# Kernel tuning notes

Hardware: AMD Instinct MI355X
Metric: run time of the kernel (lower is better)

The kernel has to match this reference:

```python
import jax, jax.numpy as jnp
import numpy as np

D_STATE = 8
HIDDEN = 256


def _neighbor_sum(x):
    # frozen depthwise 3x3 conv, all-ones kernel with zero center, padding=1
    B, C, H, W = x.shape
    xp = jnp.pad(x, ((0, 0), (0, 0), (1, 1), (1, 1)))
    full = sum(xp[:, :, di:di + H, dj:dj + W] for di in range(3) for dj in range(3))
    return full - x  # subtract center tap


def setup_inputs() -> dict:
    key = jax.random.key(0)
    ks = jax.random.split(key, 6)
    B, H, W = 4, 256, 256
    c_in = 2 * D_STATE          # 16
    c_nbr = c_in * 8            # 128
    c_out = 8 * D_STATE         # 64
    s = 0.05
    return {
        "x_cat": jax.random.normal(ks[0], (B, c_in, H, W), dtype=jnp.float32),
        "w1": jax.random.normal(ks[1], (HIDDEN, c_nbr), dtype=jnp.float32) * s,
        "w2": jax.random.normal(ks[2], (HIDDEN, HIDDEN), dtype=jnp.float32) * s,
        "w3": jax.random.normal(ks[3], (HIDDEN, HIDDEN), dtype=jnp.float32) * s,
        "w4": jax.random.normal(ks[4], (HIDDEN, HIDDEN), dtype=jnp.float32) * s,
        "w5": jax.random.normal(ks[5], (c_out, HIDDEN), dtype=jnp.float32) * s,
    }


def reference(x_cat, w1, w2, w3, w4, w5):
    B, C, H, W = x_cat.shape
    d_state = C // 2
    # depthwise stencil: each of the 8 out-channels per group is the same neighbor sum
    nbr = _neighbor_sum(x_cat)                      # [B, 2d, H, W]
    xn = jnp.repeat(nbr, 8, axis=1)                 # [B, 16d, H, W]
    # five 1x1 convs with interleaved ELU (per-pixel MLP)
    h = jax.nn.elu(jnp.einsum('bchw,oc->bohw', xn, w1))
    h = jax.nn.elu(jnp.einsum('bchw,oc->bohw', h, w2))
    h = jax.nn.elu(jnp.einsum('bchw,oc->bohw', h, w3))
    h = jax.nn.elu(jnp.einsum('bchw,oc->bohw', h, w4))
    F_int = jnp.einsum('bchw,oc->bohw', h, w5)      # [B, 8d, H, W]
    d4 = 4 * d_state
    real = F_int[:, :d4].reshape(B, 4, d_state, H, W).mean(axis=1) * 0.1
    imag = F_int[:, d4:].reshape(B, 4, d_state, H, W).mean(axis=1) * 0.1
    return jnp.concatenate([real, imag], axis=1)    # [B, 2d, H, W]
```

## Files before the change

### kernel.cpp

```cpp
#include <hip/hip_runtime.h>

typedef __attribute__((ext_vector_type(8))) short bf16x8;
typedef __attribute__((ext_vector_type(4))) float f32x4;

__device__ __forceinline__ unsigned int f2bf(float f) {
  unsigned int u = __builtin_bit_cast(unsigned int, f);
  return (u + 0x7FFFu + ((u >> 16) & 1u)) >> 16;
}
__device__ __forceinline__ float eluf(float x) {
  return x > 0.f ? x : (__expf(x) - 1.f);
}
__device__ __forceinline__ unsigned int cvt_pk_bf16(float a, float b) {
  unsigned int r;
  asm("v_cvt_pk_bf16_f32 %0, %1, %2" : "=v"(r) : "v"(a), "v"(b));
  return r;
}

__global__ __launch_bounds__(256) void prep_kernel(
    const float* __restrict__ w1, const float* __restrict__ w2,
    const float* __restrict__ w3, const float* __restrict__ w4,
    const float* __restrict__ w5, unsigned short* __restrict__ ws) {
  int idx = blockIdx.x * 256 + threadIdx.x;
  float v = 0.f;
  if (idx < 8192) {
    int mt = idx >> 9, l = (idx >> 3) & 63, j = idx & 7;
    int o = mt * 16 + (l & 15), c = (l >> 4) * 8 + j;
    if (c < 16) {
      const float* r = w1 + o * 128 + c * 8;
      v = ((r[0] + r[1]) + (r[2] + r[3])) + ((r[4] + r[5]) + (r[6] + r[7]));
    }
  } else if (idx < 204800) {
    int t = idx - 8192;
    int which = t >> 16, e = t & 65535;
    const float* w = (which == 0) ? w2 : (which == 1) ? w3 : w4;
    int mt = e >> 12, kt = (e >> 9) & 7, l = (e >> 3) & 63, j = e & 7;
    int o = mt * 16 + (l & 15), c = kt * 32 + (l >> 4) * 8 + j;
    v = w[o * 256 + c];
  } else {
    int e = idx - 204800;
    int kt = e >> 9, l = (e >> 3) & 63, j = e & 7;
    int d = l & 15, c = kt * 32 + (l >> 4) * 8 + j;
    float s = 0.f;
    if (d < 8) {
      for (int g = 0; g < 4; ++g) s += w5[(g * 8 + d) * 256 + c];
    } else {
      for (int g = 0; g < 4; ++g) s += w5[(32 + g * 8 + (d - 8)) * 256 + c];
    }
    v = 0.025f * s;
  }
  ws[idx] = (unsigned short)f2bf(v);
}

#define ACT0 0
#define BUF0 5120
#define BUF1 38912

__global__ __launch_bounds__(256, 2) void qca_kernel(
    const float* __restrict__ xcat, const unsigned short* __restrict__ wsu,
    float* __restrict__ out) {
  __shared__ __align__(16) char lds[72704];
  float* xt = reinterpret_cast<float*>(lds + BUF0);

  const int tid = threadIdx.x;
  const int w = tid >> 6, l = tid & 63;
  const int l15 = l & 15, lhi = l >> 4;

  const int tile = blockIdx.x << 6;
  const int bimg = tile >> 16;
  const int y = (tile >> 8) & 255;
  const int x0 = tile & 255;

  for (int t = tid; t < 16 * 3 * 66; t += 256) {
    int c = t / 198;
    int rem = t - c * 198;
    int rr = rem / 66;
    int xl = rem - rr * 66;
    int gy = y + rr - 1, gx = x0 + xl - 1;
    float v = 0.f;
    if (gy >= 0 && gy < 256 && gx >= 0 && gx < 256)
      v = xcat[(size_t)(bimg * 16 + c) * 65536 + gy * 256 + gx];
    xt[t] = v;
  }
  __syncthreads();

  for (int t = tid; t < 2048; t += 256) {
    int p = t & 63, c = t >> 6;
    float v = 0.f;
    if (c < 16) {
      const float* bp = xt + c * 198 + (p + 1);
      v = (bp[-1] + bp[0] + bp[1]) + (bp[65] + bp[67]) +
          (bp[131] + bp[132] + bp[133]);
    }
    reinterpret_cast<unsigned short*>(lds)[p * 40 + c] = (unsigned short)f2bf(v);
  }
  __syncthreads();

  const int lb_r = l15 * 528 + lhi * 16;
  const int lb_w = l15 * 528 + w * 128 + lhi * 8;
  const int lb_a1 = l15 * 80 + lhi * 16;

  f32x4 acc[4][4];

  auto epi = [&](int dstoff) {
#pragma unroll
    for (int mi = 0; mi < 4; ++mi)
#pragma unroll
      for (int ni = 0; ni < 4; ++ni) {
        f32x4 v = acc[mi][ni];
        unsigned int u01 = cvt_pk_bf16(eluf(v[0]), eluf(v[1]));
        unsigned int u23 = cvt_pk_bf16(eluf(v[2]), eluf(v[3]));
        *reinterpret_cast<uint2*>(lds + lb_w + (dstoff + ni * 8448 + mi * 32)) =
            uint2{u01, u23};
      }
  };

  {
#pragma unroll
    for (int mi = 0; mi < 4; ++mi)
#pragma unroll
      for (int ni = 0; ni < 4; ++ni) acc[mi][ni] = f32x4{0.f, 0.f, 0.f, 0.f};
    const bf16x8* w1v = reinterpret_cast<const bf16x8*>(wsu);
    bf16x8 a[4], bq[4];
#pragma unroll
    for (int mi = 0; mi < 4; ++mi) a[mi] = w1v[((w << 2) + mi) * 64 + l];
#pragma unroll
    for (int ni = 0; ni < 4; ++ni)
      bq[ni] = *reinterpret_cast<const bf16x8*>(lds + lb_a1 + ni * 1280);
#pragma unroll
    for (int mi = 0; mi < 4; ++mi)
#pragma unroll
      for (int ni = 0; ni < 4; ++ni)
        acc[mi][ni] = __builtin_amdgcn_mfma_f32_16x16x32_bf16(
            a[mi], bq[ni], acc[mi][ni], 0, 0, 0);
    epi(BUF1);
    __syncthreads();
  }

  auto mid = [&](int srcoff, int dstoff, const unsigned short* wbase) {
    const bf16x8* wv = reinterpret_cast<const bf16x8*>(wbase);
#pragma unroll
    for (int mi = 0; mi < 4; ++mi)
#pragma unroll
      for (int ni = 0; ni < 4; ++ni) acc[mi][ni] = f32x4{0.f, 0.f, 0.f, 0.f};
#pragma unroll
    for (int kt = 0; kt < 8; ++kt) {
      bf16x8 a[4], bq[4];
#pragma unroll
      for (int mi = 0; mi < 4; ++mi)
        a[mi] = wv[(((w << 2) + mi) * 8 + kt) * 64 + l];
#pragma unroll
      for (int ni = 0; ni < 4; ++ni)
        bq[ni] = *reinterpret_cast<const bf16x8*>(
            lds + lb_r + (srcoff + ni * 8448 + kt * 64));
#pragma unroll
      for (int mi = 0; mi < 4; ++mi)
#pragma unroll
        for (int ni = 0; ni < 4; ++ni)
          acc[mi][ni] = __builtin_amdgcn_mfma_f32_16x16x32_bf16(
              a[mi], bq[ni], acc[mi][ni], 0, 0, 0);
    }
    epi(dstoff);
    __syncthreads();
  };

  mid(BUF1, BUF0, wsu + 8192);
  mid(BUF0, BUF1, wsu + 73728);
  mid(BUF1, BUF0, wsu + 139264);

  {
    const bf16x8* w5v = reinterpret_cast<const bf16x8*>(wsu + 204800);
    f32x4 a5 = f32x4{0.f, 0.f, 0.f, 0.f};
    const int p = (w << 4) + l15;
    const int lb5 = p * 528 + lhi * 16;
#pragma unroll
    for (int kt = 0; kt < 8; ++kt) {
      bf16x8 a = w5v[kt * 64 + l];
      bf16x8 b = *reinterpret_cast<const bf16x8*>(lds + lb5 + (BUF0 + kt * 64));
      a5 = __builtin_amdgcn_mfma_f32_16x16x32_bf16(a, b, a5, 0, 0, 0);
    }
    int pix = tile + p;
    int rem = pix & 65535;
    float* op = out + (size_t)(pix >> 16) * 1048576 + rem;
#pragma unroll
    for (int r = 0; r < 4; ++r) op[(lhi * 4 + r) * 65536] = a5[r];
  }
}

extern "C" void kernel_launch(void* const* d_in, const int* in_sizes, int n_in,
                              void* d_out, int out_size, void* d_ws,
                              size_t ws_size, hipStream_t stream) {
  const float* xcat = (const float*)d_in[0];
  const float* w1 = (const float*)d_in[1];
  const float* w2 = (const float*)d_in[2];
  const float* w3 = (const float*)d_in[3];
  const float* w4 = (const float*)d_in[4];
  const float* w5 = (const float*)d_in[5];
  unsigned short* ws = (unsigned short*)d_ws;
  float* out = (float*)d_out;

  prep_kernel<<<816, 256, 0, stream>>>(w1, w2, w3, w4, w5, ws);
  qca_kernel<<<4096, 256, 0, stream>>>(xcat, ws, out);
}
```

Baseline: 169.0 us.

## Single-buffer LDS activations to raise occupancy to four blocks per CU

Replaces the ping-pong activation buffers with one in-place buffer, adding a barrier before each layer's epilogue so all reads finish before it is overwritten. This cuts LDS per block from about 71KB to 38KB and raises launch bounds to four blocks per CU, giving more waves to hide latency. In exchange each layer gets an extra __syncthreads, and the register budget per thread is tighter, which could cause spills given the 16 f32x4 accumulators.

```diff
diff --git a/kernel.cpp b/kernel.cpp
--- a/kernel.cpp
+++ b/kernel.cpp
@@ -51,15 +51,13 @@
   ws[idx] = (unsigned short)f2bf(v);
 }
 
-#define ACT0 0
-#define BUF0 5120
-#define BUF1 38912
-
-__global__ __launch_bounds__(256, 2) void qca_kernel(
+#define ACT0 33792
+
+__global__ __launch_bounds__(256, 4) void qca_kernel(
     const float* __restrict__ xcat, const unsigned short* __restrict__ wsu,
     float* __restrict__ out) {
-  __shared__ __align__(16) char lds[72704];
-  float* xt = reinterpret_cast<float*>(lds + BUF0);
+  __shared__ __align__(16) char lds[38912];
+  float* xt = reinterpret_cast<float*>(lds);
 
   const int tid = threadIdx.x;
   const int w = tid >> 6, l = tid & 63;
@@ -91,7 +89,8 @@
       v = (bp[-1] + bp[0] + bp[1]) + (bp[65] + bp[67]) +
           (bp[131] + bp[132] + bp[133]);
     }
-    reinterpret_cast<unsigned short*>(lds)[p * 40 + c] = (unsigned short)f2bf(v);
+    reinterpret_cast<unsigned short*>(lds + ACT0)[p * 40 + c] =
+        (unsigned short)f2bf(v);
   }
   __syncthreads();
 
@@ -101,7 +100,7 @@
 
   f32x4 acc[4][4];
 
-  auto epi = [&](int dstoff) {
+  auto epi = [&]() {
 #pragma unroll
     for (int mi = 0; mi < 4; ++mi)
 #pragma unroll
@@ -109,7 +108,7 @@
         f32x4 v = acc[mi][ni];
         unsigned int u01 = cvt_pk_bf16(eluf(v[0]), eluf(v[1]));
         unsigned int u23 = cvt_pk_bf16(eluf(v[2]), eluf(v[3]));
-        *reinterpret_cast<uint2*>(lds + lb_w + (dstoff + ni * 8448 + mi * 32)) =
+        *reinterpret_cast<uint2*>(lds + lb_w + (ni * 8448 + mi * 32)) =
             uint2{u01, u23};
       }
   };
@@ -125,18 +124,18 @@
     for (int mi = 0; mi < 4; ++mi) a[mi] = w1v[((w << 2) + mi) * 64 + l];
 #pragma unroll
     for (int ni = 0; ni < 4; ++ni)
-      bq[ni] = *reinterpret_cast<const bf16x8*>(lds + lb_a1 + ni * 1280);
+      bq[ni] = *reinterpret_cast<const bf16x8*>(lds + ACT0 + lb_a1 + ni * 1280);
 #pragma unroll
     for (int mi = 0; mi < 4; ++mi)
 #pragma unroll
       for (int ni = 0; ni < 4; ++ni)
         acc[mi][ni] = __builtin_amdgcn_mfma_f32_16x16x32_bf16(
             a[mi], bq[ni], acc[mi][ni], 0, 0, 0);
-    epi(BUF1);
+    epi();
     __syncthreads();
   }
 
-  auto mid = [&](int srcoff, int dstoff, const unsigned short* wbase) {
+  auto mid = [&](const unsigned short* wbase) {
     const bf16x8* wv = reinterpret_cast<const bf16x8*>(wbase);
 #pragma unroll
     for (int mi = 0; mi < 4; ++mi)
@@ -151,7 +150,7 @@
 #pragma unroll
       for (int ni = 0; ni < 4; ++ni)
         bq[ni] = *reinterpret_cast<const bf16x8*>(
-            lds + lb_r + (srcoff + ni * 8448 + kt * 64));
+            lds + lb_r + (ni * 8448 + kt * 64));
 #pragma unroll
       for (int mi = 0; mi < 4; ++mi)
 #pragma unroll
@@ -159,13 +158,14 @@
           acc[mi][ni] = __builtin_amdgcn_mfma_f32_16x16x32_bf16(
               a[mi], bq[ni], acc[mi][ni], 0, 0, 0);
     }
-    epi(dstoff);
+    __syncthreads();
+    epi();
     __syncthreads();
   };
 
-  mid(BUF1, BUF0, wsu + 8192);
-  mid(BUF0, BUF1, wsu + 73728);
-  mid(BUF1, BUF0, wsu + 139264);
+  mid(wsu + 8192);
+  mid(wsu + 73728);
+  mid(wsu + 139264);
 
   {
     const bf16x8* w5v = reinterpret_cast<const bf16x8*>(wsu + 204800);
@@ -175,7 +175,7 @@
 #pragma unroll
     for (int kt = 0; kt < 8; ++kt) {
       bf16x8 a = w5v[kt * 64 + l];
-      bf16x8 b = *reinterpret_cast<const bf16x8*>(lds + lb5 + (BUF0 + kt * 64));
+      bf16x8 b = *reinterpret_cast<const bf16x8*>(lds + lb5 + kt * 64);
       a5 = __builtin_amdgcn_mfma_f32_16x16x32_bf16(a, b, a5, 0, 0, 0);
     }
     int pix = tile + p;
```

Result: no change. 167.8 us (-0.7%).
